# Kernel optimization log

Measured on AMD Instinct MI355X. Metric: run time of the kernel, lower is better.

## Reference

```python
import jax, jax.numpy as jnp
import numpy as np

N_NODES = 4096
INPUT_DIM = 512
OUTPUT_DIM = 512
NUM_HEADS = 4
HEAD_DIM = OUTPUT_DIM // NUM_HEADS
ADJ_DENSITY = 0.01


def setup_inputs() -> dict:
    key = jax.random.key(0)
    k_x, k_adj, k_qkv, k_proj = jax.random.split(key, 4)
    x = jax.random.normal(k_x, (N_NODES, INPUT_DIM), dtype=jnp.float32)
    # sparse 0/1 adjacency, stored dense; bcoo_dot_general(adj, scores) == adj @ scores
    adj = (jax.random.uniform(k_adj, (N_NODES, N_NODES)) < ADJ_DENSITY).astype(jnp.float32)
    w_qkv = jax.random.normal(k_qkv, (3, NUM_HEADS, INPUT_DIM, HEAD_DIM), dtype=jnp.float32) * 0.01
    w_proj = jax.random.normal(k_proj, (OUTPUT_DIM, OUTPUT_DIM), dtype=jnp.float32) * 0.02
    b_proj = jnp.zeros((OUTPUT_DIM,), dtype=jnp.float32)
    return {"x": x, "adj": adj, "w_qkv": w_qkv, "w_proj": w_proj, "b_proj": b_proj}


def reference(x, adj, w_qkv, w_proj, b_proj):
    # x: [N, D]; w_qkv: [3, H, D, Hd]
    N = x.shape[0]
    q, k, v = jnp.einsum('bd,sndh->sbnh', x, w_qkv)  # each [N, H, Hd]
    scale = jnp.sqrt(jnp.asarray(k.shape[-1], x.dtype))
    scores = jnp.einsum('tnh,snh->tns', q / scale, k)       # [N, H, N]
    # bcoo_dot_general(adj, scores, (([1],[0]),([],[]))) == adj @ scores over node dim
    masked = jnp.einsum('ts,sna->tna', adj, scores)          # [N, H, N]
    attn = jax.nn.softmax(masked, axis=-1)                   # softmax over last axis
    # y = einsum('TNS,BNH->BNH', attn, v): attn reduced over T and S per head
    head_w = attn.sum(axis=(0, 2))                           # [H]
    y = v * head_w[None, :, None]                            # [N, H, Hd]
    return y.reshape(N, -1) @ w_proj + b_proj                # [N, output_dim]
```

## Files before the change

kernel.cpp:

```cpp
#include <hip/hip_runtime.h>
#include <hip/hip_bf16.h>


constexpr int NNODES = 4096;
constexpr int DIM = 512;

typedef __bf16 bf16x8 __attribute__((ext_vector_type(8)));
typedef float f32x4 __attribute__((ext_vector_type(4)));

__device__ __forceinline__ bf16x8 cvt8(const float* p) {
  const f32x4 lo = *(const f32x4*)p;
  const f32x4 hi = *(const f32x4*)(p + 4);
  bf16x8 r;
#pragma unroll
  for (int j = 0; j < 4; ++j) { r[j] = (__bf16)lo[j]; r[4 + j] = (__bf16)hi[j]; }
  return r;
}

__global__ __launch_bounds__(256) void cvt_x(
    const float* __restrict__ x, __bf16* __restrict__ xb) {
  const int t = blockIdx.x * 256 + threadIdx.x;
  *(bf16x8*)&xb[(size_t)t * 8] = cvt8(&x[(size_t)t * 8]);
}

__global__ __launch_bounds__(64) void build_Mt(
    const float* __restrict__ w_qkv,
    const float* __restrict__ w_proj,
    __bf16* __restrict__ Mt) {
  const int lane = threadIdx.x;
  const int ln = lane & 15, q = lane >> 4;
  const int m0 = blockIdx.y * 32;
  const int n0 = blockIdx.x * 32;
  const float* __restrict__ wv = w_qkv + 2 * 4 * DIM * 128;

  f32x4 acc[2][2] = {};

#pragma unroll
  for (int k0 = 0; k0 < DIM; k0 += 32) {
    const int h = k0 >> 7, hb = k0 & 127;
    bf16x8 af[2], bf[2];
#pragma unroll
    for (int mi = 0; mi < 2; ++mi) {
      float raw[8];
#pragma unroll
      for (int j = 0; j < 8; ++j)
        raw[j] = w_proj[(k0 + q * 8 + j) * DIM + (m0 + mi * 16 + ln)];
#pragma unroll
      for (int j = 0; j < 8; ++j) af[mi][j] = (__bf16)raw[j];
    }
#pragma unroll
    for (int ni = 0; ni < 2; ++ni)
      bf[ni] = cvt8(&wv[((size_t)h * DIM + (n0 + ni * 16 + ln)) * 128 + hb + q * 8]);
#pragma unroll
    for (int mi = 0; mi < 2; ++mi)
#pragma unroll
      for (int ni = 0; ni < 2; ++ni)
        acc[mi][ni] = __builtin_amdgcn_mfma_f32_16x16x32_bf16(
            af[mi], bf[ni], acc[mi][ni], 0, 0, 0);
  }

#pragma unroll
  for (int mi = 0; mi < 2; ++mi)
#pragma unroll
    for (int ni = 0; ni < 2; ++ni)
#pragma unroll
      for (int r = 0; r < 4; ++r) {
        const int o = m0 + mi * 16 + q * 4 + r;
        const int d = n0 + ni * 16 + ln;
        Mt[o * DIM + d] = (__bf16)(acc[mi][ni][r] * (float)NNODES);
      }
}

__global__ __launch_bounds__(256) void gemm_out(
    const __bf16* __restrict__ xb,
    const __bf16* __restrict__ Mt,
    const float* __restrict__ bias,
    float* __restrict__ out) {
  const int tid = threadIdx.x;
  const int wave = tid >> 6, lane = tid & 63;
  const int ln = lane & 15, q = lane >> 4;
  const int m0 = blockIdx.y * 64 + (wave >> 1) * 32;
  const int n0 = blockIdx.x * 128 + (wave & 1) * 64;

  f32x4 acc[2][4] = {};

#pragma unroll 4
  for (int k0 = 0; k0 < DIM; k0 += 32) {
    bf16x8 af[2], bf[4];
#pragma unroll
    for (int mi = 0; mi < 2; ++mi)
      af[mi] = *(const bf16x8*)&xb[(size_t)(m0 + mi * 16 + ln) * DIM + k0 + q * 8];
#pragma unroll
    for (int ni = 0; ni < 4; ++ni)
      bf[ni] = *(const bf16x8*)&Mt[(size_t)(n0 + ni * 16 + ln) * DIM + k0 + q * 8];
#pragma unroll
    for (int mi = 0; mi < 2; ++mi)
#pragma unroll
      for (int ni = 0; ni < 4; ++ni)
        acc[mi][ni] = __builtin_amdgcn_mfma_f32_16x16x32_bf16(
            af[mi], bf[ni], acc[mi][ni], 0, 0, 0);
  }

#pragma unroll
  for (int ni = 0; ni < 4; ++ni) {
    const int o = n0 + ni * 16 + ln;
    const float bj = bias[o];
#pragma unroll
    for (int mi = 0; mi < 2; ++mi)
#pragma unroll
      for (int r = 0; r < 4; ++r) {
        const int b = m0 + mi * 16 + q * 4 + r;
        out[(size_t)b * DIM + o] = acc[mi][ni][r] + bj;
      }
  }
}

extern "C" void kernel_launch(void* const* d_in, const int* in_sizes, int n_in,
                              void* d_out, int out_size, void* d_ws, size_t ws_size,
                              hipStream_t stream) {
  const float* x      = (const float*)d_in[0];
  const float* w_qkv  = (const float*)d_in[2];
  const float* w_proj = (const float*)d_in[3];
  const float* b_proj = (const float*)d_in[4];
  __bf16* Mt = (__bf16*)d_ws;
  __bf16* xb = (__bf16*)((char*)d_ws + DIM * DIM * 2);
  float* out = (float*)d_out;

  cvt_x<<<dim3(NNODES * DIM / (256 * 8)), 256, 0, stream>>>(x, xb);
  build_Mt<<<dim3(DIM / 32, DIM / 32), 64, 0, stream>>>(w_qkv, w_proj, Mt);
  gemm_out<<<dim3(DIM / 128, NNODES / 64), 256, 0, stream>>>(xb, Mt, b_proj, out);
}
```

Measured before the change: 125.4 us.

## Fuse convert, weight-fold and output GEMM into one cooperative kernel

Merges the x-to-bf16 conversion, the folded weight build and the output GEMM into a single kernel launched cooperatively with 256 blocks. A grid-wide sync separates the producer phases from the GEMM. The intent is to remove two kernel launches and the gaps between them. In exchange it pays for a grid barrier and cooperative-launch overhead, and each phase is constrained to the same 256-block grid shape.

```diff
diff --git a/kernel.cpp b/kernel.cpp
--- a/kernel.cpp
+++ b/kernel.cpp
@@ -1,5 +1,8 @@
 #include <hip/hip_runtime.h>
 #include <hip/hip_bf16.h>
+#include <hip/hip_cooperative_groups.h>
+
+namespace cg = cooperative_groups;
 
 
 constexpr int NNODES = 4096;
@@ -17,101 +20,90 @@
   return r;
 }
 
-__global__ __launch_bounds__(256) void cvt_x(
-    const float* __restrict__ x, __bf16* __restrict__ xb) {
-  const int t = blockIdx.x * 256 + threadIdx.x;
-  *(bf16x8*)&xb[(size_t)t * 8] = cvt8(&x[(size_t)t * 8]);
-}
-
-__global__ __launch_bounds__(64) void build_Mt(
+__global__ __launch_bounds__(256) void fused(
+    const float* __restrict__ x,
     const float* __restrict__ w_qkv,
     const float* __restrict__ w_proj,
-    __bf16* __restrict__ Mt) {
-  const int lane = threadIdx.x;
+    const float* __restrict__ bias,
+    __bf16* __restrict__ Mt,
+    __bf16* __restrict__ xb,
+    float* __restrict__ out) {
+  const int tid = threadIdx.x;
+  const int bid = blockIdx.x;
+  const int wave = tid >> 6, lane = tid & 63;
   const int ln = lane & 15, q = lane >> 4;
-  const int m0 = blockIdx.y * 32;
-  const int n0 = blockIdx.x * 32;
-  const float* __restrict__ wv = w_qkv + 2 * 4 * DIM * 128;
 
-  f32x4 acc[2][2] = {};
+  {
+    const int gt = bid * 256 + tid;
+#pragma unroll
+    for (int j = 0; j < 4; ++j) {
+      const size_t i8 = (size_t)(j * 65536 + gt) * 8;
+      *(bf16x8*)&xb[i8] = cvt8(&x[i8]);
+    }
+  }
 
+  {
+    const int wid = bid * 4 + wave;
+    const int o0 = (wid >> 5) * 16;
+    const int d0 = (wid & 31) * 16;
+    const float* __restrict__ wv = w_qkv + 2 * 4 * DIM * 128;
+
+    f32x4 acc = {};
 #pragma unroll
-  for (int k0 = 0; k0 < DIM; k0 += 32) {
-    const int h = k0 >> 7, hb = k0 & 127;
-    bf16x8 af[2], bf[2];
-#pragma unroll
-    for (int mi = 0; mi < 2; ++mi) {
+    for (int k0 = 0; k0 < DIM; k0 += 32) {
+      const int h = k0 >> 7, hb = k0 & 127;
       float raw[8];
 #pragma unroll
       for (int j = 0; j < 8; ++j)
-        raw[j] = w_proj[(k0 + q * 8 + j) * DIM + (m0 + mi * 16 + ln)];
+        raw[j] = w_proj[(k0 + q * 8 + j) * DIM + o0 + ln];
+      bf16x8 af, bf;
 #pragma unroll
-      for (int j = 0; j < 8; ++j) af[mi][j] = (__bf16)raw[j];
+      for (int j = 0; j < 8; ++j) af[j] = (__bf16)raw[j];
+      bf = cvt8(&wv[((size_t)h * DIM + d0 + ln) * 128 + hb + q * 8]);
+      acc = __builtin_amdgcn_mfma_f32_16x16x32_bf16(af, bf, acc, 0, 0, 0);
     }
 #pragma unroll
-    for (int ni = 0; ni < 2; ++ni)
-      bf[ni] = cvt8(&wv[((size_t)h * DIM + (n0 + ni * 16 + ln)) * 128 + hb + q * 8]);
-#pragma unroll
-    for (int mi = 0; mi < 2; ++mi)
-#pragma unroll
-      for (int ni = 0; ni < 2; ++ni)
-        acc[mi][ni] = __builtin_amdgcn_mfma_f32_16x16x32_bf16(
-            af[mi], bf[ni], acc[mi][ni], 0, 0, 0);
+    for (int r = 0; r < 4; ++r)
+      Mt[(o0 + q * 4 + r) * DIM + d0 + ln] = (__bf16)(acc[r] * (float)NNODES);
   }
 
-#pragma unroll
-  for (int mi = 0; mi < 2; ++mi)
-#pragma unroll
-    for (int ni = 0; ni < 2; ++ni)
-#pragma unroll
-      for (int r = 0; r < 4; ++r) {
-        const int o = m0 + mi * 16 + q * 4 + r;
-        const int d = n0 + ni * 16 + ln;
-        Mt[o * DIM + d] = (__bf16)(acc[mi][ni][r] * (float)NNODES);
-      }
-}
+  cg::this_grid().sync();
 
-__global__ __launch_bounds__(256) void gemm_out(
-    const __bf16* __restrict__ xb,
-    const __bf16* __restrict__ Mt,
-    const float* __restrict__ bias,
-    float* __restrict__ out) {
-  const int tid = threadIdx.x;
-  const int wave = tid >> 6, lane = tid & 63;
-  const int ln = lane & 15, q = lane >> 4;
-  const int m0 = blockIdx.y * 64 + (wave >> 1) * 32;
-  const int n0 = blockIdx.x * 128 + (wave & 1) * 64;
+  {
+    const int m0 = (bid >> 2) * 64 + (wave >> 1) * 32;
+    const int n0 = (bid & 3) * 128 + (wave & 1) * 64;
 
-  f32x4 acc[2][4] = {};
+    f32x4 acc[2][4] = {};
 
 #pragma unroll 4
-  for (int k0 = 0; k0 < DIM; k0 += 32) {
-    bf16x8 af[2], bf[4];
+    for (int k0 = 0; k0 < DIM; k0 += 32) {
+      bf16x8 af[2], bf[4];
 #pragma unroll
-    for (int mi = 0; mi < 2; ++mi)
-      af[mi] = *(const bf16x8*)&xb[(size_t)(m0 + mi * 16 + ln) * DIM + k0 + q * 8];
-#pragma unroll
-    for (int ni = 0; ni < 4; ++ni)
-      bf[ni] = *(const bf16x8*)&Mt[(size_t)(n0 + ni * 16 + ln) * DIM + k0 + q * 8];
-#pragma unroll
-    for (int mi = 0; mi < 2; ++mi)
+      for (int mi = 0; mi < 2; ++mi)
+        af[mi] = *(const bf16x8*)&xb[(size_t)(m0 + mi * 16 + ln) * DIM + k0 + q * 8];
 #pragma unroll
       for (int ni = 0; ni < 4; ++ni)
-        acc[mi][ni] = __builtin_amdgcn_mfma_f32_16x16x32_bf16(
-            af[mi], bf[ni], acc[mi][ni], 0, 0, 0);
-  }
+        bf[ni] = *(const bf16x8*)&Mt[(size_t)(n0 + ni * 16 + ln) * DIM + k0 + q * 8];
+#pragma unroll
+      for (int mi = 0; mi < 2; ++mi)
+#pragma unroll
+        for (int ni = 0; ni < 4; ++ni)
+          acc[mi][ni] = __builtin_amdgcn_mfma_f32_16x16x32_bf16(
+              af[mi], bf[ni], acc[mi][ni], 0, 0, 0);
+    }
 
 #pragma unroll
-  for (int ni = 0; ni < 4; ++ni) {
-    const int o = n0 + ni * 16 + ln;
-    const float bj = bias[o];
+    for (int ni = 0; ni < 4; ++ni) {
+      const int o = n0 + ni * 16 + ln;
+      const float bj = bias[o];
 #pragma unroll
-    for (int mi = 0; mi < 2; ++mi)
+      for (int mi = 0; mi < 2; ++mi)
 #pragma unroll
-      for (int r = 0; r < 4; ++r) {
-        const int b = m0 + mi * 16 + q * 4 + r;
-        out[(size_t)b * DIM + o] = acc[mi][ni][r] + bj;
-      }
+        for (int r = 0; r < 4; ++r) {
+          const int b = m0 + mi * 16 + q * 4 + r;
+          out[(size_t)b * DIM + o] = acc[mi][ni][r] + bj;
+        }
+    }
   }
 }
 
@@ -126,7 +118,8 @@
   __bf16* xb = (__bf16*)((char*)d_ws + DIM * DIM * 2);
   float* out = (float*)d_out;
 
-  cvt_x<<<dim3(NNODES * DIM / (256 * 8)), 256, 0, stream>>>(x, xb);
-  build_Mt<<<dim3(DIM / 32, DIM / 32), 64, 0, stream>>>(w_qkv, w_proj, Mt);
-  gemm_out<<<dim3(DIM / 128, NNODES / 64), 256, 0, stream>>>(xb, Mt, b_proj, out);
+  void* args[] = {(void*)&x, (void*)&w_qkv, (void*)&w_proj, (void*)&b_proj,
+                  (void*)&Mt, (void*)&xb, (void*)&out};
+  hipLaunchCooperativeKernel((const void*)fused, dim3(256), dim3(256),
+                             args, 0, stream);
 }
```

Result: slower. 157.0 us (+25.2%).
